# Kernel tuning notes

Measured on AMD Instinct MI355X. Metric: run time of the kernel, lower is better.

## Reference

```python
import jax, jax.numpy as jnp
import numpy as np

BS = 256
HID = 1024
ACT = 16
MEM_DIM = 512
NUM_MEM = 1024
MEM_H = 32  # sqrt(NUM_MEM)
ALPHA_T = 1.0


def setup_inputs() -> dict:
    key = jax.random.key(0)
    ks = jax.random.split(key, 16)
    w = lambda i, shape: (jax.random.normal(ks[i], shape, jnp.float32) * 0.02)
    inp = {
        "h": jax.random.normal(ks[0], (BS, HID), jnp.float32),
        "a": jax.random.uniform(ks[1], (BS, ACT), jnp.float32),
        "prev_h": jax.random.normal(ks[2], (BS, HID), jnp.float32),
        "prev_alpha": jax.random.uniform(ks[3], (BS, NUM_MEM), jnp.float32),
        "M": jax.random.normal(ks[4], (BS, NUM_MEM, MEM_DIM), jnp.float32) * 0.05,
        # get_vars_h: Linear(HID, 3*MEM_DIM)
        "Wv": w(5, (HID, 3 * MEM_DIM)), "bv": jnp.zeros((3 * MEM_DIM,), jnp.float32),
        # get_kernel: Linear(ACT, MEM_DIM) -> LeakyReLU(0.2) -> Linear(MEM_DIM, 9)
        "Wk1": w(6, (ACT, MEM_DIM)), "bk1": jnp.zeros((MEM_DIM,), jnp.float32),
        "Wk2": w(7, (MEM_DIM, 9)), "bk2": jnp.zeros((9,), jnp.float32),
        # get_gate: Linear(HID, MEM_DIM) -> LeakyReLU(0.2) -> Linear(MEM_DIM, 1) -> Sigmoid
        "Wg1": w(8, (HID, MEM_DIM)), "bg1": jnp.zeros((MEM_DIM,), jnp.float32),
        "Wg2": w(9, (MEM_DIM, 1)), "bg2": jnp.zeros((1,), jnp.float32),
    }
    return inp


def _kernel_net(x, Wk1, bk1, Wk2, bk2):
    # [bs, ACT] -> [bs, 1, 3, 3]
    k = jax.nn.leaky_relu(x @ Wk1 + bk1, 0.2) @ Wk2 + bk2
    return k.reshape(-1, 1, 3, 3)


def _dyn_conv(prev_alpha, kernels):
    # per-sample 3x3 conv: input [1, bs, 32, 32], kernel [bs, 1, 3, 3], groups=bs
    x = prev_alpha.reshape(1, BS, MEM_H, MEM_H)
    out = jax.lax.conv_general_dilated(
        x, kernels, window_strides=(1, 1), padding="SAME",
        dimension_numbers=("NCHW", "OIHW", "NCHW"), feature_group_count=BS)
    return out.reshape(BS, NUM_MEM)


def reference(h, a, prev_h, prev_alpha, M,
              Wv, bv, Wk1, bk1, Wk2, bk2, Wg1, bg1, Wg2, bg2):
    # mem_use_h=True -> memory query input is h (prev_h unused)
    kernels = _kernel_net(a, Wk1, bk1, Wk2, bk2)

    # vizdoom action masking (vectorized): if argmax(a)==0 -> a[1]=1, a[0]=0
    m = jnp.argmax(a, axis=1) == 0  # [bs]
    new_a = a.at[:, 0].set(jnp.where(m, 0.0, a[:, 0]))
    new_a = new_a.at[:, 1].set(jnp.where(m, 1.0, new_a[:, 1]))
    flipped = _kernel_net(new_a, Wk1, bk1, Wk2, bk2)[:, :, ::-1, ::-1]
    maskf = m.astype(jnp.float32)[:, None, None, None]
    kernels = (1.0 - maskf) * kernels + maskf * flipped

    # softmax_kernel=True
    kernels = jax.nn.softmax(kernels.reshape(BS, 9) / ALPHA_T, axis=1)
    kernels = kernels.reshape(BS, 1, 3, 3)

    gate = jax.nn.sigmoid(jax.nn.leaky_relu(h @ Wg1 + bg1, 0.2) @ Wg2 + bg2)  # [bs,1]

    alpha = _dyn_conv(prev_alpha, kernels)           # [bs, NUM_MEM]
    alpha = alpha * gate + prev_alpha * (1.0 - gate)

    # write (read_only=False)
    tmp = h @ Wv + bv                                 # [bs, 3*MEM_DIM]
    erase_v = jax.nn.sigmoid(tmp[:, :MEM_DIM])
    add_v = tmp[:, MEM_DIM:2 * MEM_DIM]
    other_v = tmp[:, 2 * MEM_DIM:]
    erase = alpha[:, :, None] * erase_v[:, None, :]   # [bs, NUM_MEM, MEM_DIM]
    add = alpha[:, :, None] * add_v[:, None, :]
    M_new = M * (1.0 - erase) + add

    read_v = jnp.einsum("bn,bnd->bd", alpha, M_new)   # [bs, MEM_DIM]
    return read_v, other_v, M_new, alpha
```

## Files before the change

kernel.cpp:

```cpp
#include <hip/hip_runtime.h>
#include <math.h>

#define BS 256
#define HID 1024
#define ACT 16
#define MEM_DIM 512
#define NUM_MEM 1024
#define MEM_H 32

#define OUT_READV 0
#define OUT_OTHER (BS * MEM_DIM)
#define OUT_MNEW  (2 * BS * MEM_DIM)
#define OUT_ALPHA (2 * BS * MEM_DIM + (size_t)BS * NUM_MEM * MEM_DIM)

#define WS_ERASE 0
#define WS_ADD   (BS * MEM_DIM)
#define WS_G1    (2 * BS * MEM_DIM)
#define WS_K9    (3 * BS * MEM_DIM)

typedef float v4f __attribute__((ext_vector_type(4)));

__device__ __forceinline__ float sigmoidf_(float x) { return 1.f / (1.f + expf(-x)); }
__device__ __forceinline__ float leakyf_(float x) { return x > 0.f ? x : 0.2f * x; }

__global__ __launch_bounds__(64) void knet_kernel(
    const float* __restrict__ a, const float* __restrict__ Wk1,
    const float* __restrict__ bk1, const float* __restrict__ Wk2,
    const float* __restrict__ bk2, float* __restrict__ k9out)
{
    int b = blockIdx.x;
    int t = threadIdx.x;
    __shared__ float as[ACT];
    if (t < ACT) as[t] = a[b * ACT + t];
    __syncthreads();

    float mx = as[1];
    #pragma unroll
    for (int j = 2; j < ACT; ++j) mx = fmaxf(mx, as[j]);
    bool m = as[0] >= mx;

    float po[9], pn[9];
    #pragma unroll
    for (int o = 0; o < 9; ++o) { po[o] = 0.f; pn[o] = 0.f; }

    #pragma unroll
    for (int i = 0; i < 8; ++i) {
        int u = t + 64 * i;
        float so = bk1[u], sn = bk1[u];
        #pragma unroll
        for (int j = 0; j < ACT; ++j) {
            float w  = Wk1[j * MEM_DIM + u];
            float av = as[j];
            float avn = (j == 0) ? (m ? 0.f : av)
                      : (j == 1) ? (m ? 1.f : av) : av;
            so += av * w;
            sn += avn * w;
        }
        so = leakyf_(so);
        sn = leakyf_(sn);
        #pragma unroll
        for (int o = 0; o < 9; ++o) {
            float w2 = Wk2[u * 9 + o];
            po[o] += so * w2;
            pn[o] += sn * w2;
        }
    }
    #pragma unroll
    for (int off = 32; off; off >>= 1) {
        #pragma unroll
        for (int o = 0; o < 9; ++o) {
            po[o] += __shfl_down(po[o], off, 64);
            pn[o] += __shfl_down(pn[o], off, 64);
        }
    }
    if (t == 0) {
        float k[9];
        #pragma unroll
        for (int o = 0; o < 9; ++o) {
            float ko = po[o] + bk2[o];
            float kn = pn[8 - o] + bk2[8 - o];
            k[o] = m ? kn : ko;
        }
        float kmax = k[0];
        #pragma unroll
        for (int o = 1; o < 9; ++o) kmax = fmaxf(kmax, k[o]);
        float s = 0.f;
        #pragma unroll
        for (int o = 0; o < 9; ++o) { k[o] = expf(k[o] - kmax); s += k[o]; }
        float inv = 1.f / s;
        #pragma unroll
        for (int o = 0; o < 9; ++o) k9out[b * 9 + o] = k[o] * inv;
    }
}

#define TM 32
#define TN 64
#define KC 32

__global__ __launch_bounds__(256) void gemm_fused_kernel(
    const float* __restrict__ h, const float* __restrict__ Wv,
    const float* __restrict__ Wg1, const float* __restrict__ bv,
    const float* __restrict__ bg1, float* __restrict__ ws,
    float* __restrict__ out_other)
{
    __shared__ float As[KC][TM + 1];
    __shared__ float Bs[KC][TN + 4];
    int tid = threadIdx.x;
    int n0 = blockIdx.x * TN;
    int m0 = blockIdx.y * TM;
    int tc = tid & 15, tr = tid >> 4;

    float acc[2][4];
    #pragma unroll
    for (int j = 0; j < 2; ++j)
        #pragma unroll
        for (int i = 0; i < 4; ++i) acc[j][i] = 0.f;

    int a_m  = tid >> 3;
    int a_k4 = (tid & 7) * 4;
    int b_n4 = (tid & 15) * 4;
    int b_k  = tid >> 4;
    const bool isWv = (n0 < 3 * MEM_DIM);

    for (int k0 = 0; k0 < HID; k0 += KC) {
        float4 av4 = *(const float4*)&h[(size_t)(m0 + a_m) * HID + k0 + a_k4];
        As[a_k4 + 0][a_m] = av4.x;
        As[a_k4 + 1][a_m] = av4.y;
        As[a_k4 + 2][a_m] = av4.z;
        As[a_k4 + 3][a_m] = av4.w;
        #pragma unroll
        for (int p = 0; p < 2; ++p) {
            int kk = b_k + p * 16;
            float4 bv4;
            if (isWv)
                bv4 = *(const float4*)&Wv[(size_t)(k0 + kk) * (3 * MEM_DIM) + n0 + b_n4];
            else
                bv4 = *(const float4*)&Wg1[(size_t)(k0 + kk) * MEM_DIM + (n0 - 3 * MEM_DIM) + b_n4];
            *(float4*)&Bs[kk][b_n4] = bv4;
        }
        __syncthreads();
        #pragma unroll
        for (int k = 0; k < KC; ++k) {
            float a0 = As[k][tr * 2 + 0];
            float a1 = As[k][tr * 2 + 1];
            float4 b4 = *(float4*)&Bs[k][tc * 4];
            acc[0][0] += a0 * b4.x; acc[0][1] += a0 * b4.y;
            acc[0][2] += a0 * b4.z; acc[0][3] += a0 * b4.w;
            acc[1][0] += a1 * b4.x; acc[1][1] += a1 * b4.y;
            acc[1][2] += a1 * b4.z; acc[1][3] += a1 * b4.w;
        }
        __syncthreads();
    }

    int seg = n0 >> 9;
    #pragma unroll
    for (int j = 0; j < 2; ++j) {
        int r = m0 + tr * 2 + j;
        #pragma unroll
        for (int i = 0; i < 4; ++i) {
            int c = n0 + tc * 4 + i;
            float v = acc[j][i];
            if (seg < 3) v += bv[c]; else v += bg1[c - 3 * MEM_DIM];
            if (seg == 0)      ws[WS_ERASE + r * MEM_DIM + c]               = sigmoidf_(v);
            else if (seg == 1) ws[WS_ADD   + r * MEM_DIM + (c - MEM_DIM)]   = v;
            else if (seg == 2) out_other[r * MEM_DIM + (c - 2 * MEM_DIM)]   = v;
            else               ws[WS_G1    + r * MEM_DIM + (c - 3 * MEM_DIM)] = leakyf_(v);
        }
    }
}

__global__ __launch_bounds__(256) void conv_gate_kernel(
    const float* __restrict__ prev_alpha, const float* __restrict__ g1,
    const float* __restrict__ Wg2, const float* __restrict__ bg2,
    const float* __restrict__ k9, float* __restrict__ alpha_out)
{
    int b = blockIdx.x;
    int t = threadIdx.x;
    __shared__ float pa[NUM_MEM];
    __shared__ float ksh[9];
    __shared__ float red[4];
    __shared__ float gsh;

    float p = g1[b * MEM_DIM + t] * Wg2[t]
            + g1[b * MEM_DIM + 256 + t] * Wg2[256 + t];
    #pragma unroll
    for (int off = 32; off; off >>= 1) p += __shfl_down(p, off, 64);
    if ((t & 63) == 0) red[t >> 6] = p;

    *(float4*)&pa[t * 4] = *(const float4*)&prev_alpha[b * NUM_MEM + t * 4];
    if (t < 9) ksh[t] = k9[b * 9 + t];
    __syncthreads();
    if (t == 0) gsh = sigmoidf_(red[0] + red[1] + red[2] + red[3] + bg2[0]);
    __syncthreads();
    float gate = gsh;

    #pragma unroll
    for (int q = 0; q < 4; ++q) {
        int c = t * 4 + q;
        int i = c >> 5, j = c & 31;
        float s = 0.f;
        #pragma unroll
        for (int ki = 0; ki < 3; ++ki) {
            int ii = i + ki - 1;
            if (ii < 0 || ii >= MEM_H) continue;
            #pragma unroll
            for (int kj = 0; kj < 3; ++kj) {
                int jj = j + kj - 1;
                if (jj < 0 || jj >= MEM_H) continue;
                s += pa[ii * MEM_H + jj] * ksh[ki * 3 + kj];
            }
        }
        alpha_out[b * NUM_MEM + c] = s * gate + pa[c] * (1.f - gate);
    }
}

__global__ __launch_bounds__(256) void update_kernel(
    const float* __restrict__ M, const float* __restrict__ alpha,
    const float* __restrict__ erase, const float* __restrict__ add,
    float* __restrict__ M_new, float* __restrict__ read_v)
{
    int b  = blockIdx.x;
    int nc = blockIdx.y;
    int t  = threadIdx.x;
    int n_off = t >> 7;
    int d = (t & 127) * 4;

    __shared__ float al[256];
    al[t] = alpha[b * NUM_MEM + nc * 256 + t];
    __syncthreads();

    v4f e  = *(const v4f*)(erase + b * MEM_DIM + d);
    v4f ad = *(const v4f*)(add   + b * MEM_DIM + d);
    const float* Mb = M     + (size_t)b * NUM_MEM * MEM_DIM + (size_t)(nc * 256) * MEM_DIM + d;
    float*       Ob = M_new + (size_t)b * NUM_MEM * MEM_DIM + (size_t)(nc * 256) * MEM_DIM + d;

    v4f acc = 0.f;
    #pragma unroll 8
    for (int ni = n_off; ni < 256; ni += 2) {
        float av = al[ni];
        v4f m4 = __builtin_nontemporal_load((const v4f*)(Mb + (size_t)ni * MEM_DIM));
        v4f mn = m4 * (1.f - av * e) + av * ad;
        __builtin_nontemporal_store(mn, (v4f*)(Ob + (size_t)ni * MEM_DIM));
        acc += av * mn;
    }
    float* rv = read_v + b * MEM_DIM + d;
    atomicAdd(rv + 0, acc.x);
    atomicAdd(rv + 1, acc.y);
    atomicAdd(rv + 2, acc.z);
    atomicAdd(rv + 3, acc.w);
}

extern "C" void kernel_launch(void* const* d_in, const int* in_sizes, int n_in,
                              void* d_out, int out_size, void* d_ws, size_t ws_size,
                              hipStream_t stream)
{
    const float* h          = (const float*)d_in[0];
    const float* a          = (const float*)d_in[1];
    const float* prev_alpha = (const float*)d_in[3];
    const float* M          = (const float*)d_in[4];
    const float* Wv         = (const float*)d_in[5];
    const float* bv         = (const float*)d_in[6];
    const float* Wk1        = (const float*)d_in[7];
    const float* bk1        = (const float*)d_in[8];
    const float* Wk2        = (const float*)d_in[9];
    const float* bk2        = (const float*)d_in[10];
    const float* Wg1        = (const float*)d_in[11];
    const float* bg1        = (const float*)d_in[12];
    const float* Wg2        = (const float*)d_in[13];
    const float* bg2        = (const float*)d_in[14];

    float* out = (float*)d_out;
    float* ws  = (float*)d_ws;

    float* out_readv = out + OUT_READV;
    float* out_other = out + OUT_OTHER;
    float* out_mnew  = out + OUT_MNEW;
    float* out_alpha = out + OUT_ALPHA;

    hipMemsetAsync(out_readv, 0, (size_t)BS * MEM_DIM * sizeof(float), stream);

    knet_kernel<<<BS, 64, 0, stream>>>(a, Wk1, bk1, Wk2, bk2, ws + WS_K9);
    gemm_fused_kernel<<<dim3(2048 / TN, BS / TM), 256, 0, stream>>>(
        h, Wv, Wg1, bv, bg1, ws, out_other);
    conv_gate_kernel<<<BS, 256, 0, stream>>>(
        prev_alpha, ws + WS_G1, Wg2, bg2, ws + WS_K9, out_alpha);
    update_kernel<<<dim3(BS, 4), 256, 0, stream>>>(
        M, out_alpha, ws + WS_ERASE, ws + WS_ADD, out_mnew, out_readv);
}
```

Before: 968.8 us.

## Fuse kernel-net, conv/gate and memory update into one kernel; drop atomics

Merges the kernel-net, conv+gate and memory update stages into a single kernel whose blocks are split by batch and a 128-wide column chunk. Each block recomputes the 3x3 softmax kernel, the gate and alpha using dedicated thread groups, then streams all 1024 memory rows for its column chunk. read_v is reduced in shared memory and written directly, which removes the memset and the atomicAdds. This cuts three launches and the global round-trips of alpha and k9, at the cost of computing the kernel-net and conv redundantly in each of the four column blocks per batch.

```diff
diff --git a/kernel.cpp b/kernel.cpp
--- a/kernel.cpp
+++ b/kernel.cpp
@@ -16,82 +16,11 @@
 #define WS_ERASE 0
 #define WS_ADD   (BS * MEM_DIM)
 #define WS_G1    (2 * BS * MEM_DIM)
-#define WS_K9    (3 * BS * MEM_DIM)
 
 typedef float v4f __attribute__((ext_vector_type(4)));
 
 __device__ __forceinline__ float sigmoidf_(float x) { return 1.f / (1.f + expf(-x)); }
 __device__ __forceinline__ float leakyf_(float x) { return x > 0.f ? x : 0.2f * x; }
-
-__global__ __launch_bounds__(64) void knet_kernel(
-    const float* __restrict__ a, const float* __restrict__ Wk1,
-    const float* __restrict__ bk1, const float* __restrict__ Wk2,
-    const float* __restrict__ bk2, float* __restrict__ k9out)
-{
-    int b = blockIdx.x;
-    int t = threadIdx.x;
-    __shared__ float as[ACT];
-    if (t < ACT) as[t] = a[b * ACT + t];
-    __syncthreads();
-
-    float mx = as[1];
-    #pragma unroll
-    for (int j = 2; j < ACT; ++j) mx = fmaxf(mx, as[j]);
-    bool m = as[0] >= mx;
-
-    float po[9], pn[9];
-    #pragma unroll
-    for (int o = 0; o < 9; ++o) { po[o] = 0.f; pn[o] = 0.f; }
-
-    #pragma unroll
-    for (int i = 0; i < 8; ++i) {
-        int u = t + 64 * i;
-        float so = bk1[u], sn = bk1[u];
-        #pragma unroll
-        for (int j = 0; j < ACT; ++j) {
-            float w  = Wk1[j * MEM_DIM + u];
-            float av = as[j];
-            float avn = (j == 0) ? (m ? 0.f : av)
-                      : (j == 1) ? (m ? 1.f : av) : av;
-            so += av * w;
-            sn += avn * w;
-        }
-        so = leakyf_(so);
-        sn = leakyf_(sn);
-        #pragma unroll
-        for (int o = 0; o < 9; ++o) {
-            float w2 = Wk2[u * 9 + o];
-            po[o] += so * w2;
-            pn[o] += sn * w2;
-        }
-    }
-    #pragma unroll
-    for (int off = 32; off; off >>= 1) {
-        #pragma unroll
-        for (int o = 0; o < 9; ++o) {
-            po[o] += __shfl_down(po[o], off, 64);
-            pn[o] += __shfl_down(pn[o], off, 64);
-        }
-    }
-    if (t == 0) {
-        float k[9];
-        #pragma unroll
-        for (int o = 0; o < 9; ++o) {
-            float ko = po[o] + bk2[o];
-            float kn = pn[8 - o] + bk2[8 - o];
-            k[o] = m ? kn : ko;
-        }
-        float kmax = k[0];
-        #pragma unroll
-        for (int o = 1; o < 9; ++o) kmax = fmaxf(kmax, k[o]);
-        float s = 0.f;
-        #pragma unroll
-        for (int o = 0; o < 9; ++o) { k[o] = expf(k[o] - kmax); s += k[o]; }
-        float inv = 1.f / s;
-        #pragma unroll
-        for (int o = 0; o < 9; ++o) k9out[b * 9 + o] = k[o] * inv;
-    }
-}
 
 #define TM 32
 #define TN 64
@@ -169,31 +98,111 @@
     }
 }
 
-__global__ __launch_bounds__(256) void conv_gate_kernel(
-    const float* __restrict__ prev_alpha, const float* __restrict__ g1,
-    const float* __restrict__ Wg2, const float* __restrict__ bg2,
-    const float* __restrict__ k9, float* __restrict__ alpha_out)
+__global__ __launch_bounds__(256) void update_fused_kernel(
+    const float* __restrict__ a, const float* __restrict__ Wk1,
+    const float* __restrict__ bk1, const float* __restrict__ Wk2,
+    const float* __restrict__ bk2,
+    const float* __restrict__ prev_alpha,
+    const float* __restrict__ g1, const float* __restrict__ Wg2,
+    const float* __restrict__ bg2,
+    const float* __restrict__ M,
+    const float* __restrict__ erase, const float* __restrict__ add,
+    float* __restrict__ M_new, float* __restrict__ read_v,
+    float* __restrict__ alpha_out)
 {
-    int b = blockIdx.x;
-    int t = threadIdx.x;
-    __shared__ float pa[NUM_MEM];
+    int b  = blockIdx.x;
+    int dc = blockIdx.y;
+    int t  = threadIdx.x;
+
+    __shared__ __align__(16) float pa[NUM_MEM];
+    __shared__ __align__(16) float al[NUM_MEM];
     __shared__ float ksh[9];
-    __shared__ float red[4];
     __shared__ float gsh;
 
-    float p = g1[b * MEM_DIM + t] * Wg2[t]
-            + g1[b * MEM_DIM + 256 + t] * Wg2[256 + t];
-    #pragma unroll
-    for (int off = 32; off; off >>= 1) p += __shfl_down(p, off, 64);
-    if ((t & 63) == 0) red[t >> 6] = p;
-
-    *(float4*)&pa[t * 4] = *(const float4*)&prev_alpha[b * NUM_MEM + t * 4];
-    if (t < 9) ksh[t] = k9[b * 9 + t];
+    int dl = (t & 31) * 4;
+    int d  = dc * 128 + dl;
+    v4f e  = *(const v4f*)(erase + b * MEM_DIM + d);
+    v4f ad = *(const v4f*)(add   + b * MEM_DIM + d);
+
+    if (t < 64) {
+        float as_[ACT];
+        #pragma unroll
+        for (int j = 0; j < ACT; ++j) as_[j] = a[b * ACT + j];
+        float mx = as_[1];
+        #pragma unroll
+        for (int j = 2; j < ACT; ++j) mx = fmaxf(mx, as_[j]);
+        bool m = as_[0] >= mx;
+
+        float po[9], pn[9];
+        #pragma unroll
+        for (int o = 0; o < 9; ++o) { po[o] = 0.f; pn[o] = 0.f; }
+
+        #pragma unroll
+        for (int i = 0; i < 8; ++i) {
+            int u = t + 64 * i;
+            float so = bk1[u], sn = bk1[u];
+            #pragma unroll
+            for (int j = 0; j < ACT; ++j) {
+                float w  = Wk1[j * MEM_DIM + u];
+                float av = as_[j];
+                float avn = (j == 0) ? (m ? 0.f : av)
+                          : (j == 1) ? (m ? 1.f : av) : av;
+                so += av * w;
+                sn += avn * w;
+            }
+            so = leakyf_(so);
+            sn = leakyf_(sn);
+            #pragma unroll
+            for (int o = 0; o < 9; ++o) {
+                float w2 = Wk2[u * 9 + o];
+                po[o] += so * w2;
+                pn[o] += sn * w2;
+            }
+        }
+        #pragma unroll
+        for (int off = 32; off; off >>= 1) {
+            #pragma unroll
+            for (int o = 0; o < 9; ++o) {
+                po[o] += __shfl_down(po[o], off, 64);
+                pn[o] += __shfl_down(pn[o], off, 64);
+            }
+        }
+        if (t == 0) {
+            float k[9];
+            #pragma unroll
+            for (int o = 0; o < 9; ++o) {
+                float ko = po[o] + bk2[o];
+                float kn = pn[8 - o] + bk2[8 - o];
+                k[o] = m ? kn : ko;
+            }
+            float kmax = k[0];
+            #pragma unroll
+            for (int o = 1; o < 9; ++o) kmax = fmaxf(kmax, k[o]);
+            float s = 0.f;
+            #pragma unroll
+            for (int o = 0; o < 9; ++o) { k[o] = expf(k[o] - kmax); s += k[o]; }
+            float inv = 1.f / s;
+            #pragma unroll
+            for (int o = 0; o < 9; ++o) ksh[o] = k[o] * inv;
+        }
+    } else if (t < 128) {
+        int l = t - 64;
+        float p = 0.f;
+        #pragma unroll
+        for (int k = 0; k < 8; ++k)
+            p += g1[b * MEM_DIM + l + 64 * k] * Wg2[l + 64 * k];
+        #pragma unroll
+        for (int off = 32; off; off >>= 1) p += __shfl_down(p, off, 64);
+        if (l == 0) gsh = sigmoidf_(p + bg2[0]);
+    } else {
+        int i0 = (t - 128) * 8;
+        *(float4*)&pa[i0]     = *(const float4*)&prev_alpha[(size_t)b * NUM_MEM + i0];
+        *(float4*)&pa[i0 + 4] = *(const float4*)&prev_alpha[(size_t)b * NUM_MEM + i0 + 4];
+    }
     __syncthreads();
-    if (t == 0) gsh = sigmoidf_(red[0] + red[1] + red[2] + red[3] + bg2[0]);
-    __syncthreads();
+
     float gate = gsh;
-
+    v4f outv;
     #pragma unroll
     for (int q = 0; q < 4; ++q) {
         int c = t * 4 + q;
@@ -210,44 +219,38 @@
                 s += pa[ii * MEM_H + jj] * ksh[ki * 3 + kj];
             }
         }
-        alpha_out[b * NUM_MEM + c] = s * gate + pa[c] * (1.f - gate);
-    }
-}
-
-__global__ __launch_bounds__(256) void update_kernel(
-    const float* __restrict__ M, const float* __restrict__ alpha,
-    const float* __restrict__ erase, const float* __restrict__ add,
-    float* __restrict__ M_new, float* __restrict__ read_v)
-{
-    int b  = blockIdx.x;
-    int nc = blockIdx.y;
-    int t  = threadIdx.x;
-    int n_off = t >> 7;
-    int d = (t & 127) * 4;
-
-    __shared__ float al[256];
-    al[t] = alpha[b * NUM_MEM + nc * 256 + t];
+        float v = s * gate + pa[c] * (1.f - gate);
+        al[c] = v;
+        outv[q] = v;
+    }
+    if (dc == 0)
+        *(v4f*)&alpha_out[(size_t)b * NUM_MEM + t * 4] = outv;
     __syncthreads();
 
-    v4f e  = *(const v4f*)(erase + b * MEM_DIM + d);
-    v4f ad = *(const v4f*)(add   + b * MEM_DIM + d);
-    const float* Mb = M     + (size_t)b * NUM_MEM * MEM_DIM + (size_t)(nc * 256) * MEM_DIM + d;
-    float*       Ob = M_new + (size_t)b * NUM_MEM * MEM_DIM + (size_t)(nc * 256) * MEM_DIM + d;
+    const float* Mb = M     + (size_t)b * NUM_MEM * MEM_DIM + d;
+    float*       Ob = M_new + (size_t)b * NUM_MEM * MEM_DIM + d;
+    const float* alp = &al[(t >> 5) * 128];
+    Mb += (size_t)(t >> 5) * 128 * MEM_DIM;
+    Ob += (size_t)(t >> 5) * 128 * MEM_DIM;
 
     v4f acc = 0.f;
     #pragma unroll 8
-    for (int ni = n_off; ni < 256; ni += 2) {
-        float av = al[ni];
-        v4f m4 = __builtin_nontemporal_load((const v4f*)(Mb + (size_t)ni * MEM_DIM));
+    for (int i = 0; i < 128; ++i) {
+        float av = alp[i];
+        v4f m4 = __builtin_nontemporal_load((const v4f*)(Mb + (size_t)i * MEM_DIM));
         v4f mn = m4 * (1.f - av * e) + av * ad;
-        __builtin_nontemporal_store(mn, (v4f*)(Ob + (size_t)ni * MEM_DIM));
+        __builtin_nontemporal_store(mn, (v4f*)(Ob + (size_t)i * MEM_DIM));
         acc += av * mn;
     }
-    float* rv = read_v + b * MEM_DIM + d;
-    atomicAdd(rv + 0, acc.x);
-    atomicAdd(rv + 1, acc.y);
-    atomicAdd(rv + 2, acc.z);
-    atomicAdd(rv + 3, acc.w);
+
+    *(v4f*)&pa[t * 4] = acc;
+    __syncthreads();
+    if (t < 32) {
+        v4f s = *(v4f*)&pa[t * 4];
+        #pragma unroll
+        for (int j = 1; j < 8; ++j) s += *(v4f*)&pa[(t + 32 * j) * 4];
+        *(v4f*)(read_v + (size_t)b * MEM_DIM + dc * 128 + t * 4) = s;
+    }
 }
 
 extern "C" void kernel_launch(void* const* d_in, const int* in_sizes, int n_in,
@@ -277,13 +280,12 @@
     float* out_mnew  = out + OUT_MNEW;
     float* out_alpha = out + OUT_ALPHA;
 
-    hipMemsetAsync(out_readv, 0, (size_t)BS * MEM_DIM * sizeof(float), stream);
-
-    knet_kernel<<<BS, 64, 0, stream>>>(a, Wk1, bk1, Wk2, bk2, ws + WS_K9);
     gemm_fused_kernel<<<dim3(2048 / TN, BS / TM), 256, 0, stream>>>(
         h, Wv, Wg1, bv, bg1, ws, out_other);
-    conv_gate_kernel<<<BS, 256, 0, stream>>>(
-        prev_alpha, ws + WS_G1, Wg2, bg2, ws + WS_K9, out_alpha);
-    update_kernel<<<dim3(BS, 4), 256, 0, stream>>>(
-        M, out_alpha, ws + WS_ERASE, ws + WS_ADD, out_mnew, out_readv);
+
+    update_fused_kernel<<<dim3(BS, 4), 256, 0, stream>>>(
+        a, Wk1, bk1, Wk2, bk2, prev_alpha,
+        ws + WS_G1, Wg2, bg2, M,
+        ws + WS_ERASE, ws + WS_ADD,
+        out_mnew, out_readv, out_alpha);
 }
```

After: 960.5 us. About the same (-0.9%).
